# Kernel optimization log

Hardware: AMD Instinct MI355X
Metric: run time of the kernel (lower is better)

Reference implementation:

```python
import jax, jax.numpy as jnp
import numpy as np


def _gcn_norm(edge_index, num_nodes):
    # PyG GCNConv default: add self-loops, symmetric normalization.
    src, dst = edge_index[0], edge_index[1]
    loop = jnp.arange(num_nodes, dtype=edge_index.dtype)
    src = jnp.concatenate([src, loop])
    dst = jnp.concatenate([dst, loop])
    deg = jax.ops.segment_sum(jnp.ones_like(dst, dtype=jnp.float32), dst,
                              num_segments=num_nodes)
    dinv = jnp.where(deg > 0, jax.lax.rsqrt(deg), 0.0)
    norm = dinv[src] * dinv[dst]  # [E + N]
    return src, dst, norm


def _gcn_conv(x, src, dst, norm, W, b):
    h = x @ W                      # [N, F_out]
    msg = h[src] * norm[:, None]   # gather + scale, [E+N, F_out]
    agg = jax.ops.segment_sum(msg, dst, num_segments=x.shape[0])
    return agg + b


def reference(x, edge_index, W1, b1, W2, b2, Wfc, bfc):
    N = x.shape[0]
    src, dst, norm = _gcn_norm(edge_index, N)
    h = jax.nn.relu(_gcn_conv(x, src, dst, norm, W1, b1))
    h = jax.nn.relu(_gcn_conv(h, src, dst, norm, W2, b2))
    return h @ Wfc + bfc  # [N, 2]


def setup_inputs() -> dict:
    N, E, D, OUT = 50000, 800000, 128, 2
    key = jax.random.key(0)
    ks = jax.random.split(key, 6)
    s = 1.0 / np.sqrt(D)
    return {
        "x": jax.random.normal(ks[0], (N, D), dtype=jnp.float32),
        "edge_index": jax.random.randint(ks[1], (2, E), 0, N, dtype=jnp.int32),
        "W1": jax.random.normal(ks[2], (D, D), dtype=jnp.float32) * s,
        "b1": jnp.zeros((D,), dtype=jnp.float32),
        "W2": jax.random.normal(ks[3], (D, D), dtype=jnp.float32) * s,
        "b2": jnp.zeros((D,), dtype=jnp.float32),
        "Wfc": jax.random.normal(ks[4], (D, OUT), dtype=jnp.float32) * s,
        "bfc": jnp.zeros((OUT,), dtype=jnp.float32),
    }
```

## Files before the change

### kernel.cpp

```cpp
#include <hip/hip_runtime.h>
#include <hip/hip_fp16.h>

#define D 128
#define GEMM_TM 64
#define EDGE_BLOCKS 2048
#define CAP 64

typedef _Float16 f16x8 __attribute__((ext_vector_type(8)));
typedef float f32x4 __attribute__((ext_vector_type(4)));

__global__ void k_prep(int4* __restrict__ fill4, int n4,
                       const float* __restrict__ W2,
                       f16x8* __restrict__ wt2, int zb) {
    int b = blockIdx.x;
    if (b < zb) {
        int i = b * 256 + threadIdx.x;
        if (i < n4) fill4[i] = make_int4(0, 0, 0, 0);
        return;
    }
    int u = (b - zb) * 256 + threadIdx.x;
    int c = u & 127;
    int k0 = (u >> 7) * 8;
    f16x8 v;
#pragma unroll
    for (int j = 0; j < 8; ++j) v[j] = (_Float16)W2[(k0 + j) * D + c];
    wt2[u] = v;
}

__global__ void k_dinv(const int* __restrict__ fill, float* __restrict__ dinv,
                       unsigned short* __restrict__ col,
                       __half* __restrict__ t1, __half* __restrict__ t2, int N) {
    int i = blockIdx.x * 256 + threadIdx.x;
    if (i < N) {
        int deg = fill[i];
        if (deg > CAP) deg = CAP;
        dinv[i] = rsqrtf((float)(deg + 1));
        int dpad = (deg + 15) & ~15;
        for (int p = deg; p < dpad; ++p)
            col[(size_t)i * CAP + p] = (unsigned short)N;
    } else if (i == N) {
        dinv[N] = 0.f;
    }
    if (i < D) {
        t1[(size_t)N * D + i] = __ushort_as_half((unsigned short)0);
        t2[(size_t)N * D + i] = __ushort_as_half((unsigned short)0);
    }
}

__device__ __forceinline__ void stage_wt(const float* __restrict__ W, f16x8* wt) {
#pragma unroll
    for (int i = 0; i < 8; ++i) {
        int u = i * 256 + threadIdx.x;
        int c = u & 127;
        int k0 = (u >> 7) * 8;
        f16x8 v;
#pragma unroll
        for (int j = 0; j < 8; ++j) v[j] = (_Float16)W[(k0 + j) * D + c];
        wt[u] = v;
    }
}

__device__ __forceinline__ void mfma_rows(const f16x8 af[4], const f16x8* wt,
                                          __half* __restrict__ Y,
                                          int row_base, int N, int lane,
                                          const float sc[4]) {
    int kg = lane >> 4;
    int c15 = lane & 15;
#pragma unroll
    for (int ct = 0; ct < 8; ++ct) {
        f32x4 acc = {0.f, 0.f, 0.f, 0.f};
#pragma unroll
        for (int ks = 0; ks < 4; ++ks) {
            f16x8 bf = wt[(ks * 4 + kg) * 128 + ct * 16 + c15];
            acc = __builtin_amdgcn_mfma_f32_16x16x32_f16(af[ks], bf, acc, 0, 0, 0);
        }
        int c = ct * 16 + c15;
#pragma unroll
        for (int r = 0; r < 4; ++r) {
            int grow = row_base + kg * 4 + r;
            if (grow < N) Y[(size_t)grow * D + c] = __float2half(sc[r] * acc[r]);
        }
    }
}

__global__ __launch_bounds__(256) void k_gemm1_bin(const float* __restrict__ X,
                                                   const float* __restrict__ W1,
                                                   __half* __restrict__ T1,
                                                   int gblocks, int NV,
                                                   const int* __restrict__ src,
                                                   const int* __restrict__ dst,
                                                   int* __restrict__ fill,
                                                   unsigned short* __restrict__ col,
                                                   int E) {
    __shared__ f16x8 wt[2048];
    int b = blockIdx.x;
    if (b >= gblocks) {
        int w = b - gblocks;
        int r = b & 7;
        int lo = (r * NV) >> 3;
        int hi = ((r + 1) * NV) >> 3;
        int idx = (w >> 3) * 256 + threadIdx.x;
        int stride4 = (EDGE_BLOCKS / 8) * 256 * 4;
        for (int e4 = idx * 4; e4 < E; e4 += stride4) {
            if (e4 + 4 <= E) {
                int4 dv = *(const int4*)(dst + e4);
                int4 sv = *(const int4*)(src + e4);
#pragma unroll
                for (int j = 0; j < 4; ++j) {
                    int d = (j == 0) ? dv.x : (j == 1) ? dv.y : (j == 2) ? dv.z : dv.w;
                    int s = (j == 0) ? sv.x : (j == 1) ? sv.y : (j == 2) ? sv.z : sv.w;
                    if (d >= lo && d < hi) {
                        int pos = atomicAdd(&fill[d], 1);
                        if (pos < CAP) col[(size_t)d * CAP + pos] = (unsigned short)s;
                    }
                }
            } else {
                for (int e = e4; e < E; ++e) {
                    int d = dst[e];
                    if (d >= lo && d < hi) {
                        int s = src[e];
                        int pos = atomicAdd(&fill[d], 1);
                        if (pos < CAP) col[(size_t)d * CAP + pos] = (unsigned short)s;
                    }
                }
            }
        }
        return;
    }
    stage_wt(W1, wt);
    __syncthreads();

    int lane = threadIdx.x & 63, w = threadIdx.x >> 6;
    int tile_row = b * GEMM_TM + w * 16;
    int ar = tile_row + (lane & 15);
    const float* xr = X + (size_t)(ar < NV ? ar : NV - 1) * D;
    int kg = lane >> 4;
    f16x8 af[4];
#pragma unroll
    for (int ks = 0; ks < 4; ++ks) {
        float4 lo4 = *(const float4*)(xr + ks * 32 + kg * 8);
        float4 hi4 = *(const float4*)(xr + ks * 32 + kg * 8 + 4);
        f16x8 v = {(_Float16)lo4.x, (_Float16)lo4.y, (_Float16)lo4.z, (_Float16)lo4.w,
                   (_Float16)hi4.x, (_Float16)hi4.y, (_Float16)hi4.z, (_Float16)hi4.w};
        af[ks] = v;
    }
    const float one4[4] = {1.f, 1.f, 1.f, 1.f};
    mfma_rows(af, wt, T1, tile_row, NV, lane, one4);
}

__global__ __launch_bounds__(256) void k_gemm2(const __half* __restrict__ H,
                                               const f16x8* __restrict__ wt2,
                                               const float* __restrict__ dinv,
                                               __half* __restrict__ T2, int N) {
    int lane = threadIdx.x & 63, w = threadIdx.x >> 6;
    int tile_row = blockIdx.x * GEMM_TM + w * 16;
    int ar = tile_row + (lane & 15);
    const __half* hr = H + (size_t)(ar < N ? ar : N - 1) * D;
    int kg = lane >> 4;
    f16x8 af[4];
#pragma unroll
    for (int ks = 0; ks < 4; ++ks)
        af[ks] = *(const f16x8*)(hr + ks * 32 + kg * 8);
    float sc[4];
#pragma unroll
    for (int r = 0; r < 4; ++r) {
        int grow = tile_row + kg * 4 + r;
        sc[r] = (grow < N) ? dinv[grow] : 1.f;
    }
    mfma_rows(af, wt2, T2, tile_row, N, lane, sc);
}

template <int MODE>
__device__ __forceinline__ void agg_core(const __half* __restrict__ T,
                                         const float* __restrict__ dinv,
                                         const unsigned short* __restrict__ col,
                                         int n, int lane, int deg,
                                         float acc[8]) {
    int l4 = lane & 15;
    int g = lane >> 4;
#pragma unroll
    for (int j = 0; j < 8; ++j) acc[j] = 0.f;
    int base = n * CAP;
    int dcap = deg < CAP ? deg : CAP;
    int dpad = (dcap + 15) & ~15;

    for (int it = 0; it < dpad; it += 16) {
        int e = base + it + g;
        int s0 = (int)col[e];
        int s1 = (int)col[e + 4];
        int s2 = (int)col[e + 8];
        int s3 = (int)col[e + 12];
        float w0, w1, w2, w3;
        if (MODE == 0) {
            w0 = dinv[s0]; w1 = dinv[s1]; w2 = dinv[s2]; w3 = dinv[s3];
        } else {
            w0 = w1 = w2 = w3 = 1.f;
        }
        f16x8 v0 = *(const f16x8*)(T + (size_t)s0 * D + l4 * 8);
        f16x8 v1 = *(const f16x8*)(T + (size_t)s1 * D + l4 * 8);
        f16x8 v2 = *(const f16x8*)(T + (size_t)s2 * D + l4 * 8);
        f16x8 v3 = *(const f16x8*)(T + (size_t)s3 * D + l4 * 8);
#pragma unroll
        for (int j = 0; j < 8; ++j) {
            acc[j] = fmaf(w0, (float)v0[j], acc[j]);
            acc[j] = fmaf(w1, (float)v1[j], acc[j]);
            acc[j] = fmaf(w2, (float)v2[j], acc[j]);
            acc[j] = fmaf(w3, (float)v3[j], acc[j]);
        }
    }
#pragma unroll
    for (int j = 0; j < 8; ++j) {
        acc[j] += __shfl_down(acc[j], 32);
        acc[j] += __shfl_down(acc[j], 16);
    }
}

__global__ __launch_bounds__(256) void agg_relu(const __half* __restrict__ T,
                                                const int* __restrict__ fill,
                                                const float* __restrict__ dinv,
                                                const unsigned short* __restrict__ col,
                                                const float* __restrict__ bias,
                                                __half* __restrict__ H, int N) {
    int n = (blockIdx.x * blockDim.x + threadIdx.x) >> 6;
    int lane = threadIdx.x & 63;
    if (n >= N) return;
    n = __builtin_amdgcn_readfirstlane(n);
    int deg = fill[n];
    float dn = dinv[n];
    float acc[8];
    agg_core<0>(T, dinv, col, n, lane, deg, acc);
    if (lane < 16) {
        int l4 = lane;
        f16x8 self = *(const f16x8*)(T + (size_t)n * D + l4 * 8);
        f32x4 b0 = *(const f32x4*)(bias + l4 * 8);
        f32x4 b1 = *(const f32x4*)(bias + l4 * 8 + 4);
        f16x8 o;
#pragma unroll
        for (int j = 0; j < 8; ++j) {
            float t = acc[j] + dn * (float)self[j];
            float bj = (j < 4) ? b0[j] : b1[j - 4];
            o[j] = (_Float16)fmaxf(fmaf(dn, t, bj), 0.f);
        }
        *(f16x8*)(H + (size_t)n * D + l4 * 8) = o;
    }
}

__global__ __launch_bounds__(256) void agg_fc(const __half* __restrict__ T,
                                              const int* __restrict__ fill,
                                              const float* __restrict__ dinv,
                                              const unsigned short* __restrict__ col,
                                              const float* __restrict__ b2,
                                              const float* __restrict__ Wfc,
                                              const float* __restrict__ bfc,
                                              float* __restrict__ out, int N) {
    int n = (blockIdx.x * blockDim.x + threadIdx.x) >> 6;
    int lane = threadIdx.x & 63;
    if (n >= N) return;
    n = __builtin_amdgcn_readfirstlane(n);
    int deg = fill[n];
    float dn = dinv[n];
    float acc[8];
    agg_core<1>(T, dinv, col, n, lane, deg, acc);
    int l4 = lane & 15;
    f16x8 self = *(const f16x8*)(T + (size_t)n * D + l4 * 8);
    f32x4 b0 = *(const f32x4*)(b2 + l4 * 8);
    f32x4 b1 = *(const f32x4*)(b2 + l4 * 8 + 4);
    float o0 = 0.f, o1 = 0.f;
#pragma unroll
    for (int j = 0; j < 8; ++j) {
        float t = acc[j] + (float)self[j];
        float bj = (j < 4) ? b0[j] : b1[j - 4];
        float h = fmaxf(fmaf(dn, t, bj), 0.f);
        float2 wf = ((const float2*)Wfc)[l4 * 8 + j];
        o0 = fmaf(h, wf.x, o0);
        o1 = fmaf(h, wf.y, o1);
    }
#pragma unroll
    for (int off = 8; off > 0; off >>= 1) {
        o0 += __shfl_xor(o0, off);
        o1 += __shfl_xor(o1, off);
    }
    if (lane == 0) {
        out[(size_t)n * 2 + 0] = o0 + bfc[0];
        out[(size_t)n * 2 + 1] = o1 + bfc[1];
    }
}


extern "C" void kernel_launch(void* const* d_in, const int* in_sizes, int n_in,
                              void* d_out, int out_size, void* d_ws, size_t ws_size,
                              hipStream_t stream) {
    const float* x   = (const float*)d_in[0];
    const int* ei    = (const int*)d_in[1];
    const float* W1  = (const float*)d_in[2];
    const float* b1  = (const float*)d_in[3];
    const float* W2  = (const float*)d_in[4];
    const float* b2  = (const float*)d_in[5];
    const float* Wfc = (const float*)d_in[6];
    const float* bfc = (const float*)d_in[7];
    float* out = (float*)d_out;

    const int N = in_sizes[0] / D;
    const int E = in_sizes[1] / 2;
    const int* src = ei;
    const int* dst = ei + E;

    f16x8* wt2  = (f16x8*)d_ws;
    __half* t1  = (__half*)(wt2 + 2048);
    __half* h16 = t1 + (size_t)(N + 1) * D;
    __half* t2  = h16 + (size_t)N * D;
    int* fill   = (int*)(t2 + (size_t)(N + 1) * D);
    float* dinv = (float*)(fill + N);
    unsigned short* col = (unsigned short*)(dinv + N + 1);

    int n4 = (N + 3) / 4;
    int zb = (n4 + 255) / 256;
    k_prep<<<zb + 8, 256, 0, stream>>>((int4*)fill, n4, W2, wt2, zb);

    int gblocks = (int)((N + GEMM_TM - 1) / GEMM_TM);

    k_gemm1_bin<<<gblocks + EDGE_BLOCKS, 256, 0, stream>>>(
        x, W1, t1, gblocks, N, src, dst, fill, col, E);

    int nb1 = (N + 1 + 255) / 256;
    k_dinv<<<nb1, 256, 0, stream>>>(fill, dinv, col, t1, t2, N);

    int ablocks = (N + 3) / 4;
    agg_relu<<<ablocks, 256, 0, stream>>>(t1, fill, dinv, col, b1, h16, N);

    k_gemm2<<<gblocks, 256, 0, stream>>>(h16, wt2, dinv, t2, N);

    agg_fc<<<ablocks, 256, 0, stream>>>(t2, fill, dinv, col, b2, Wfc, bfc, out, N);
}
```

Baseline: 127.6 us.

## Replace global-atomic CSR binning with two-pass queue and LDS bucket sort

```diff
diff --git a/kernel.cpp b/kernel.cpp
--- a/kernel.cpp
+++ b/kernel.cpp
@@ -5,46 +5,35 @@
 #define GEMM_TM 64
 #define EDGE_BLOCKS 2048
 #define CAP 64
+#define QCAP 131072
 
 typedef _Float16 f16x8 __attribute__((ext_vector_type(8)));
 typedef float f32x4 __attribute__((ext_vector_type(4)));
-
-__global__ void k_prep(int4* __restrict__ fill4, int n4,
+typedef unsigned int u32;
+
+__global__ void k_prep(int* __restrict__ qcur,
+                       float* __restrict__ dinv,
+                       __half* __restrict__ t1, __half* __restrict__ t2,
                        const float* __restrict__ W2,
-                       f16x8* __restrict__ wt2, int zb) {
+                       f16x8* __restrict__ wt2, int NV) {
     int b = blockIdx.x;
-    if (b < zb) {
-        int i = b * 256 + threadIdx.x;
-        if (i < n4) fill4[i] = make_int4(0, 0, 0, 0);
+    if (b == 0) {
+        int t = threadIdx.x;
+        if (t < 8) qcur[t] = 0;
+        if (t < 64) {
+            ((int*)(t1 + (size_t)NV * D))[t] = 0;
+            ((int*)(t2 + (size_t)NV * D))[t] = 0;
+        }
+        if (t == 64) dinv[NV] = 0.f;
         return;
     }
-    int u = (b - zb) * 256 + threadIdx.x;
+    int u = (b - 1) * 256 + threadIdx.x;
     int c = u & 127;
     int k0 = (u >> 7) * 8;
     f16x8 v;
 #pragma unroll
     for (int j = 0; j < 8; ++j) v[j] = (_Float16)W2[(k0 + j) * D + c];
     wt2[u] = v;
-}
-
-__global__ void k_dinv(const int* __restrict__ fill, float* __restrict__ dinv,
-                       unsigned short* __restrict__ col,
-                       __half* __restrict__ t1, __half* __restrict__ t2, int N) {
-    int i = blockIdx.x * 256 + threadIdx.x;
-    if (i < N) {
-        int deg = fill[i];
-        if (deg > CAP) deg = CAP;
-        dinv[i] = rsqrtf((float)(deg + 1));
-        int dpad = (deg + 15) & ~15;
-        for (int p = deg; p < dpad; ++p)
-            col[(size_t)i * CAP + p] = (unsigned short)N;
-    } else if (i == N) {
-        dinv[N] = 0.f;
-    }
-    if (i < D) {
-        t1[(size_t)N * D + i] = __ushort_as_half((unsigned short)0);
-        t2[(size_t)N * D + i] = __ushort_as_half((unsigned short)0);
-    }
 }
 
 __device__ __forceinline__ void stage_wt(const float* __restrict__ W, f16x8* wt) {
@@ -83,50 +72,74 @@
     }
 }
 
-__global__ __launch_bounds__(256) void k_gemm1_bin(const float* __restrict__ X,
-                                                   const float* __restrict__ W1,
-                                                   __half* __restrict__ T1,
-                                                   int gblocks, int NV,
-                                                   const int* __restrict__ src,
-                                                   const int* __restrict__ dst,
-                                                   int* __restrict__ fill,
-                                                   unsigned short* __restrict__ col,
-                                                   int E) {
-    __shared__ f16x8 wt[2048];
+__global__ __launch_bounds__(256) void k_gemm1_binA(const float* __restrict__ X,
+                                                    const float* __restrict__ W1,
+                                                    __half* __restrict__ T1,
+                                                    int gblocks, int NV, int RWID,
+                                                    const int* __restrict__ src,
+                                                    const int* __restrict__ dst,
+                                                    int* __restrict__ qcur,
+                                                    u32* __restrict__ queue,
+                                                    int E) {
+    __shared__ __align__(16) char lds_raw[32768];
     int b = blockIdx.x;
     if (b >= gblocks) {
         int w = b - gblocks;
-        int r = b & 7;
-        int lo = (r * NV) >> 3;
-        int hi = ((r + 1) * NV) >> 3;
-        int idx = (w >> 3) * 256 + threadIdx.x;
-        int stride4 = (EDGE_BLOCKS / 8) * 256 * 4;
-        for (int e4 = idx * 4; e4 < E; e4 += stride4) {
-            if (e4 + 4 <= E) {
-                int4 dv = *(const int4*)(dst + e4);
-                int4 sv = *(const int4*)(src + e4);
-#pragma unroll
-                for (int j = 0; j < 4; ++j) {
-                    int d = (j == 0) ? dv.x : (j == 1) ? dv.y : (j == 2) ? dv.z : dv.w;
-                    int s = (j == 0) ? sv.x : (j == 1) ? sv.y : (j == 2) ? sv.z : sv.w;
-                    if (d >= lo && d < hi) {
-                        int pos = atomicAdd(&fill[d], 1);
-                        if (pos < CAP) col[(size_t)d * CAP + pos] = (unsigned short)s;
+        int r = w & 7;
+        int lo = r * RWID;
+        int hi = min(lo + RWID, NV);
+        int g = w >> 3;
+        const int ce = ((E + 255) >> 8 + 0) ;
+        int ce8 = (((E + 255) >> 8) + 7) & ~7;
+        int e0 = g * ce8;
+        int e1 = min(e0 + ce8, E);
+        __shared__ int ecnt, gbase;
+        u32* ebuf = (u32*)lds_raw;
+        for (int tb = e0; tb < e1; tb += 2048) {
+            if (threadIdx.x == 0) ecnt = 0;
+            __syncthreads();
+            int te = min(tb + 2048, e1);
+            int my = tb + threadIdx.x * 8;
+#pragma unroll
+            for (int k = 0; k < 8; k += 4) {
+                int e4 = my + k;
+                if (e4 + 4 <= te) {
+                    int4 dv = *(const int4*)(dst + e4);
+                    int4 sv = *(const int4*)(src + e4);
+#pragma unroll
+                    for (int j = 0; j < 4; ++j) {
+                        int d = (j == 0) ? dv.x : (j == 1) ? dv.y : (j == 2) ? dv.z : dv.w;
+                        int s = (j == 0) ? sv.x : (j == 1) ? sv.y : (j == 2) ? sv.z : sv.w;
+                        if (d >= lo && d < hi) {
+                            int p = atomicAdd(&ecnt, 1);
+                            ebuf[p] = ((u32)d << 16) | (u32)s;
+                        }
                     }
-                }
-            } else {
-                for (int e = e4; e < E; ++e) {
-                    int d = dst[e];
-                    if (d >= lo && d < hi) {
-                        int s = src[e];
-                        int pos = atomicAdd(&fill[d], 1);
-                        if (pos < CAP) col[(size_t)d * CAP + pos] = (unsigned short)s;
+                } else {
+                    for (int e = e4; e < te && e < e4 + 4; ++e) {
+                        int d = dst[e];
+                        if (d >= lo && d < hi) {
+                            int s = src[e];
+                            int p = atomicAdd(&ecnt, 1);
+                            ebuf[p] = ((u32)d << 16) | (u32)s;
+                        }
                     }
                 }
             }
+            __syncthreads();
+            if (threadIdx.x == 0) gbase = atomicAdd(&qcur[r], ecnt);
+            __syncthreads();
+            u32* q = queue + (size_t)r * QCAP;
+            int cnt = ecnt, base = gbase;
+            for (int i = threadIdx.x; i < cnt; i += 256) {
+                int pos = base + i;
+                if (pos < QCAP) q[pos] = ebuf[i];
+            }
+            __syncthreads();
         }
         return;
     }
+    f16x8* wt = (f16x8*)lds_raw;
     stage_wt(W1, wt);
     __syncthreads();
 
@@ -146,6 +159,49 @@
     }
     const float one4[4] = {1.f, 1.f, 1.f, 1.f};
     mfma_rows(af, wt, T1, tile_row, NV, lane, one4);
+}
+
+__global__ __launch_bounds__(256) void k_binB(const u32* __restrict__ queue,
+                                              const int* __restrict__ qcur,
+                                              unsigned short* __restrict__ col,
+                                              int* __restrict__ fill,
+                                              float* __restrict__ dinv,
+                                              int NV, int RWID) {
+    __shared__ unsigned short colbuf[256 * CAP];
+    __shared__ int cnt[256];
+    int b = blockIdx.x;
+    int r = b & 7;
+    int wi = b >> 3;
+    int n0 = r * RWID + wi * 256;
+
+    int nvpair = (NV & 0xFFFF) | (NV << 16);
+    for (int i = threadIdx.x; i < 256 * CAP / 2; i += 256)
+        ((int*)colbuf)[i] = nvpair;
+    cnt[threadIdx.x] = 0;
+    __syncthreads();
+
+    int qlen = min(qcur[r], QCAP);
+    const u32* q = queue + (size_t)r * QCAP;
+    for (int i = threadIdx.x; i < qlen; i += 256) {
+        u32 ent = q[i];
+        int li = (int)(ent >> 16) - n0;
+        if ((unsigned)li < 256u) {
+            int pos = atomicAdd(&cnt[li], 1);
+            if (pos < CAP) colbuf[li * CAP + pos] = (unsigned short)(ent & 0xFFFFu);
+        }
+    }
+    __syncthreads();
+
+    int n = n0 + threadIdx.x;
+    if (n < NV) {
+        int deg = cnt[threadIdx.x];
+        if (deg > CAP) deg = CAP;
+        fill[n] = deg;
+        dinv[n] = rsqrtf((float)(deg + 1));
+    }
+    int4* dp = (int4*)(col + (size_t)n0 * CAP);
+    const int4* sp = (const int4*)colbuf;
+    for (int i = threadIdx.x; i < 2048; i += 256) dp[i] = sp[i];
 }
 
 __global__ __launch_bounds__(256) void k_gemm2(const __half* __restrict__ H,
@@ -305,25 +361,27 @@
     const int* src = ei;
     const int* dst = ei + E;
 
+    const int RWID = ((((N + 7) / 8) + 255) / 256) * 256;
+    const int WPR  = RWID / 256;
+
     f16x8* wt2  = (f16x8*)d_ws;
     __half* t1  = (__half*)(wt2 + 2048);
     __half* h16 = t1 + (size_t)(N + 1) * D;
     __half* t2  = h16 + (size_t)N * D;
     int* fill   = (int*)(t2 + (size_t)(N + 1) * D);
     float* dinv = (float*)(fill + N);
-    unsigned short* col = (unsigned short*)(dinv + N + 1);
-
-    int n4 = (N + 3) / 4;
-    int zb = (n4 + 255) / 256;
-    k_prep<<<zb + 8, 256, 0, stream>>>((int4*)fill, n4, W2, wt2, zb);
-
-    int gblocks = (int)((N + GEMM_TM - 1) / GEMM_TM);
-
-    k_gemm1_bin<<<gblocks + EDGE_BLOCKS, 256, 0, stream>>>(
-        x, W1, t1, gblocks, N, src, dst, fill, col, E);
-
-    int nb1 = (N + 1 + 255) / 256;
-    k_dinv<<<nb1, 256, 0, stream>>>(fill, dinv, col, t1, t2, N);
+    int* qcur   = (int*)(dinv + N + 4);
+    u32* queue  = (u32*)(qcur + 8);
+    unsigned short* col = (unsigned short*)(queue + (size_t)8 * QCAP);
+
+    k_prep<<<9, 256, 0, stream>>>(qcur, dinv, t1, t2, W2, wt2, N);
+
+    int gblocks = (N + GEMM_TM - 1) / GEMM_TM;
+
+    k_gemm1_binA<<<gblocks + EDGE_BLOCKS, 256, 0, stream>>>(
+        x, W1, t1, gblocks, N, RWID, src, dst, qcur, queue, E);
+
+    k_binB<<<8 * WPR, 256, 0, stream>>>(queue, qcur, col, fill, dinv, N, RWID);
 
     int ablocks = (N + 3) / 4;
     agg_relu<<<ablocks, 256, 0, stream>>>(t1, fill, dinv, col, b1, h16, N);
```

Measured after the change: 251.7 us. +97.2%, slower.
